# Kernel optimization log

Measured on AMD Instinct MI355X. Metric: run time of the kernel, lower is better.

The kernel has to match this reference:

```python
import jax, jax.numpy as jnp
import numpy as np

EPS = 1e-5

@jax.custom_vjp
def sign_ste(x):
    # binarize to {-1, +1}; sign(0) maps to +1 as in most binary-net impls
    return jnp.where(x >= 0, 1.0, -1.0).astype(x.dtype)

def _sign_fwd(x):
    return sign_ste(x), x

def _sign_bwd(x, g):
    # straight-through estimator with hardtanh clipping
    return (g * (jnp.abs(x) <= 1.0).astype(g.dtype),)

sign_ste.defvjp(_sign_fwd, _sign_bwd)


def setup_inputs() -> dict:
    key = jax.random.key(0)
    k1, k2, k3 = jax.random.split(key, 3)
    N, Cin, Cout = 65536, 1024, 1024
    return {
        "x": jax.random.normal(k1, (N, Cin), dtype=jnp.float32),
        "gamma": jnp.ones((Cin,), dtype=jnp.float32),
        "beta": jnp.zeros((Cin,), dtype=jnp.float32),
        "W": jax.random.normal(k2, (Cout, Cin), dtype=jnp.float32) * 0.03,
        "b": jnp.zeros((Cout,), dtype=jnp.float32),
        "scale": jnp.ones((Cout,), dtype=jnp.float32),
        "alpha": jnp.float32(0.25),
    }


def reference(x, gamma, beta, W, b, scale, alpha):
    # 1) BatchNorm1d centering (training-mode batch statistics over nodes)
    mu = jnp.mean(x, axis=0)
    var = jnp.var(x, axis=0)
    xh = (x - mu) * jax.lax.rsqrt(var + EPS) * gamma + beta
    # 2) STE binarize activations
    xq = sign_ste(xh)
    # 3) binary linear: sign(W) GEMM + bias  -> [N, Cout]
    wq = sign_ste(W)
    y = jnp.einsum('nc,oc->no', xq, wq) + b
    # 4) learned per-channel rescale
    y = y * scale
    # 5) PReLU
    return jnp.where(y > 0, y, alpha * y)
```

## Files before the change

### kernel.cpp

```cpp
#include <hip/hip_runtime.h>
#include <stdint.h>
#include <math.h>

#define NROWS 65536
#define CIN   1024
#define COUT  1024
#define KW    16
#define BN_EPS 1e-5

static constexpr size_t OFF_PSUM = 0;
static constexpr size_t OFF_PSQ  = 524288;
static constexpr size_t OFF_MU   = 1048576;
static constexpr size_t OFF_INV  = 1048576 + 4096;
static constexpr size_t OFF_WB   = 1048576 + 65536;
static constexpr size_t OFF_AB   = 1310720;

__global__ __launch_bounds__(256) void k_stats_partial(
    const float* __restrict__ x, double* __restrict__ psum, double* __restrict__ psq) {
  int c  = blockIdx.x * 256 + threadIdx.x;
  size_t r0 = (size_t)blockIdx.y * 1024;
  const float* p = x + r0 * CIN + c;
  double s = 0.0, q = 0.0;
  for (int r = 0; r < 1024; ++r) {
    double v = (double)p[(size_t)r * CIN];
    s += v;
    q = fma(v, v, q);
  }
  psum[(size_t)blockIdx.y * CIN + c] = s;
  psq [(size_t)blockIdx.y * CIN + c] = q;
}

__global__ __launch_bounds__(256) void k_stats_final(
    const double* __restrict__ psum, const double* __restrict__ psq,
    float* __restrict__ mu, float* __restrict__ inv) {
  int c = blockIdx.x * 256 + threadIdx.x;
  double s = 0.0, q = 0.0;
  for (int p = 0; p < 64; ++p) {
    s += psum[(size_t)p * CIN + c];
    q += psq [(size_t)p * CIN + c];
  }
  double mean = s / (double)NROWS;
  double var  = q / (double)NROWS - mean * mean;
  mu[c]  = (float)mean;
  inv[c] = (float)(1.0 / sqrt(var + (double)BN_EPS));
}

__global__ __launch_bounds__(256) void k_binarize_x(
    const float* __restrict__ x, const float* __restrict__ mu,
    const float* __restrict__ inv, const float* __restrict__ gamma,
    const float* __restrict__ beta, uint64_t* __restrict__ Abits) {
  int n    = blockIdx.x;
  int tid  = threadIdx.x;
  int lane = tid & 63;
  int wave = tid >> 6;
  const float* row = x + (size_t)n * CIN;
  #pragma unroll
  for (int j = 0; j < 4; ++j) {
    int c = j * 256 + tid;
    float xh = ((row[c] - mu[c]) * inv[c]) * gamma[c] + beta[c];
    uint64_t m = __ballot(xh >= 0.0f);
    if (lane == 0) Abits[(size_t)n * KW + j * 4 + wave] = m;
  }
}

__global__ __launch_bounds__(256) void k_binarize_w(
    const float* __restrict__ W, uint64_t* __restrict__ Wbits) {
  int o    = blockIdx.x;
  int tid  = threadIdx.x;
  int lane = tid & 63;
  int wave = tid >> 6;
  const float* row = W + (size_t)o * CIN;
  #pragma unroll
  for (int j = 0; j < 4; ++j) {
    int c = j * 256 + tid;
    uint64_t m = __ballot(row[c] >= 0.0f);
    if (lane == 0) Wbits[(size_t)o * KW + j * 4 + wave] = m;
  }
}

__global__ __launch_bounds__(256) void k_bingemm(
    const uint64_t* __restrict__ Abits, const uint64_t* __restrict__ Wbits,
    const float* __restrict__ bias, const float* __restrict__ scale,
    const float* __restrict__ alphaPtr, float* __restrict__ out) {
  int o = blockIdx.x * 256 + threadIdx.x;

  uint64_t B[KW];
  #pragma unroll
  for (int j = 0; j < KW; ++j) B[j] = Wbits[(size_t)o * KW + j];

  float alpha = alphaPtr[0];
  float sc = scale[o];
  float c2 = -2.0f * sc;
  float c1 = (1024.0f + bias[o]) * sc;

  int n0 = blockIdx.y * 64;
  for (int r = 0; r < 64; ++r) {
    int n = n0 + r;
    const uint64_t* A = Abits + (size_t)n * KW;
    int d0 = 0, d1 = 0, d2 = 0, d3 = 0;
    #pragma unroll
    for (int j = 0; j < KW; j += 4) {
      d0 += __popcll(A[j + 0] ^ B[j + 0]);
      d1 += __popcll(A[j + 1] ^ B[j + 1]);
      d2 += __popcll(A[j + 2] ^ B[j + 2]);
      d3 += __popcll(A[j + 3] ^ B[j + 3]);
    }
    int d = (d0 + d1) + (d2 + d3);
    float y = fmaf((float)d, c2, c1);
    out[(size_t)n * COUT + o] = y > 0.0f ? y : alpha * y;
  }
}

extern "C" void kernel_launch(void* const* d_in, const int* in_sizes, int n_in,
                              void* d_out, int out_size, void* d_ws, size_t ws_size,
                              hipStream_t stream) {
  const float* x     = (const float*)d_in[0];
  const float* gamma = (const float*)d_in[1];
  const float* beta  = (const float*)d_in[2];
  const float* W     = (const float*)d_in[3];
  const float* b     = (const float*)d_in[4];
  const float* scale = (const float*)d_in[5];
  const float* alpha = (const float*)d_in[6];
  float* out = (float*)d_out;

  char* ws = (char*)d_ws;
  double*   psum  = (double*)(ws + OFF_PSUM);
  double*   psq   = (double*)(ws + OFF_PSQ);
  float*    mu    = (float*)(ws + OFF_MU);
  float*    inv   = (float*)(ws + OFF_INV);
  uint64_t* Wbits = (uint64_t*)(ws + OFF_WB);
  uint64_t* Abits = (uint64_t*)(ws + OFF_AB);

  k_stats_partial<<<dim3(CIN / 256, NROWS / 1024), 256, 0, stream>>>(x, psum, psq);
  k_stats_final<<<dim3(CIN / 256), 256, 0, stream>>>(psum, psq, mu, inv);
  k_binarize_w<<<dim3(COUT), 256, 0, stream>>>(W, Wbits);
  k_binarize_x<<<dim3(NROWS), 256, 0, stream>>>(x, mu, inv, gamma, beta, Abits);
  k_bingemm<<<dim3(COUT / 256, NROWS / 64), 256, 0, stream>>>(
      Abits, Wbits, b, scale, alpha, out);
}
```

Measured before the change: 633.0 us.

## Vectorize stats and binarize kernels, use scalar constant loads for GEMM rows

```diff
diff --git a/kernel.cpp b/kernel.cpp
--- a/kernel.cpp
+++ b/kernel.cpp
@@ -5,109 +5,162 @@
 #define NROWS 65536
 #define CIN   1024
 #define COUT  1024
-#define KW    16
 #define BN_EPS 1e-5
 
+
 static constexpr size_t OFF_PSUM = 0;
-static constexpr size_t OFF_PSQ  = 524288;
-static constexpr size_t OFF_MU   = 1048576;
-static constexpr size_t OFF_INV  = 1048576 + 4096;
-static constexpr size_t OFF_WB   = 1048576 + 65536;
-static constexpr size_t OFF_AB   = 1310720;
+static constexpr size_t OFF_PSQ  = 2u * 1024 * 1024;
+static constexpr size_t OFF_MU   = 4u * 1024 * 1024;
+static constexpr size_t OFF_INV  = 4u * 1024 * 1024 + 4096;
+static constexpr size_t OFF_WB   = 5u * 1024 * 1024;
+static constexpr size_t OFF_AB   = 6u * 1024 * 1024;
+
+typedef uint64_t u64x2 __attribute__((ext_vector_type(2)));
+typedef uint32_t u32x4 __attribute__((ext_vector_type(4)));
+typedef const u32x4 __attribute__((address_space(4)))* c4p;
 
 __global__ __launch_bounds__(256) void k_stats_partial(
     const float* __restrict__ x, double* __restrict__ psum, double* __restrict__ psq) {
-  int c  = blockIdx.x * 256 + threadIdx.x;
-  size_t r0 = (size_t)blockIdx.y * 1024;
-  const float* p = x + r0 * CIN + c;
-  double s = 0.0, q = 0.0;
-  for (int r = 0; r < 1024; ++r) {
-    double v = (double)p[(size_t)r * CIN];
-    s += v;
-    q = fma(v, v, q);
+  int tid = threadIdx.x;
+  size_t r0 = (size_t)blockIdx.x * 256;
+  const float4* xp = (const float4*)x + r0 * 256 + tid;
+  double s0 = 0, s1 = 0, s2 = 0, s3 = 0;
+  double q0 = 0, q1 = 0, q2 = 0, q3 = 0;
+  for (int r = 0; r < 256; r += 8) {
+    float4 v[8];
+#pragma unroll
+    for (int u = 0; u < 8; ++u) v[u] = xp[(size_t)(r + u) * 256];
+#pragma unroll
+    for (int u = 0; u < 8; ++u) {
+      double a = (double)v[u].x, b = (double)v[u].y;
+      double c = (double)v[u].z, d = (double)v[u].w;
+      s0 += a; q0 = fma(a, a, q0);
+      s1 += b; q1 = fma(b, b, q1);
+      s2 += c; q2 = fma(c, c, q2);
+      s3 += d; q3 = fma(d, d, q3);
+    }
   }
-  psum[(size_t)blockIdx.y * CIN + c] = s;
-  psq [(size_t)blockIdx.y * CIN + c] = q;
+  size_t base = (size_t)blockIdx.x * CIN + (size_t)tid * 4;
+  double2* ps = (double2*)(psum + base);
+  ps[0] = make_double2(s0, s1);
+  ps[1] = make_double2(s2, s3);
+  double2* pq = (double2*)(psq + base);
+  pq[0] = make_double2(q0, q1);
+  pq[1] = make_double2(q2, q3);
 }
 
 __global__ __launch_bounds__(256) void k_stats_final(
     const double* __restrict__ psum, const double* __restrict__ psq,
     float* __restrict__ mu, float* __restrict__ inv) {
-  int c = blockIdx.x * 256 + threadIdx.x;
-  double s = 0.0, q = 0.0;
-  for (int p = 0; p < 64; ++p) {
-    s += psum[(size_t)p * CIN + c];
-    q += psq [(size_t)p * CIN + c];
+  __shared__ double sd[4][64];
+  __shared__ double sq[4][64];
+  int tid = threadIdx.x, lane = tid & 63, g = tid >> 6;
+  int col = blockIdx.x * 64 + lane;
+  double s = 0, q = 0;
+  for (int i = 0; i < 64; ++i) {
+    size_t chunk = (size_t)(g * 64 + i);
+    s += psum[chunk * CIN + col];
+    q += psq [chunk * CIN + col];
   }
-  double mean = s / (double)NROWS;
-  double var  = q / (double)NROWS - mean * mean;
-  mu[c]  = (float)mean;
-  inv[c] = (float)(1.0 / sqrt(var + (double)BN_EPS));
+  sd[g][lane] = s;
+  sq[g][lane] = q;
+  __syncthreads();
+  if (g == 0) {
+    s = sd[0][lane] + sd[1][lane] + sd[2][lane] + sd[3][lane];
+    q = sq[0][lane] + sq[1][lane] + sq[2][lane] + sq[3][lane];
+    double mean = s / (double)NROWS;
+    double var  = q / (double)NROWS - mean * mean;
+    mu[col]  = (float)mean;
+    inv[col] = (float)(1.0 / sqrt(var + (double)BN_EPS));
+  }
 }
 
 __global__ __launch_bounds__(256) void k_binarize_x(
     const float* __restrict__ x, const float* __restrict__ mu,
     const float* __restrict__ inv, const float* __restrict__ gamma,
     const float* __restrict__ beta, uint64_t* __restrict__ Abits) {
-  int n    = blockIdx.x;
-  int tid  = threadIdx.x;
-  int lane = tid & 63;
-  int wave = tid >> 6;
-  const float* row = x + (size_t)n * CIN;
-  #pragma unroll
-  for (int j = 0; j < 4; ++j) {
-    int c = j * 256 + tid;
-    float xh = ((row[c] - mu[c]) * inv[c]) * gamma[c] + beta[c];
-    uint64_t m = __ballot(xh >= 0.0f);
-    if (lane == 0) Abits[(size_t)n * KW + j * 4 + wave] = m;
+  int tid = threadIdx.x, lane = tid & 63, wv = tid >> 6;
+  float4 M  = ((const float4*)mu)[tid];
+  float4 I  = ((const float4*)inv)[tid];
+  float4 G  = ((const float4*)gamma)[tid];
+  float4 Bt = ((const float4*)beta)[tid];
+  size_t n0 = (size_t)blockIdx.x * 8;
+  const float4* xp = (const float4*)x + n0 * 256 + tid;
+  for (int r = 0; r < 8; ++r) {
+    float4 v = xp[(size_t)r * 256];
+    float h0 = ((v.x - M.x) * I.x) * G.x + Bt.x;
+    float h1 = ((v.y - M.y) * I.y) * G.y + Bt.y;
+    float h2 = ((v.z - M.z) * I.z) * G.z + Bt.z;
+    float h3 = ((v.w - M.w) * I.w) * G.w + Bt.w;
+    uint64_t b0 = __ballot(h0 >= 0.0f);
+    uint64_t b1 = __ballot(h1 >= 0.0f);
+    uint64_t b2 = __ballot(h2 >= 0.0f);
+    uint64_t b3 = __ballot(h3 >= 0.0f);
+    uint64_t t0 = b0, t1 = b1;
+    if (lane == 1) { t0 = b2; t1 = b3; }
+    if (lane < 2) {
+      u64x2 val; val.x = t0; val.y = t1;
+      *(u64x2*)(Abits + (n0 + r) * 16 + wv * 4 + lane * 2) = val;
+    }
   }
 }
 
 __global__ __launch_bounds__(256) void k_binarize_w(
     const float* __restrict__ W, uint64_t* __restrict__ Wbits) {
-  int o    = blockIdx.x;
-  int tid  = threadIdx.x;
-  int lane = tid & 63;
-  int wave = tid >> 6;
-  const float* row = W + (size_t)o * CIN;
-  #pragma unroll
-  for (int j = 0; j < 4; ++j) {
-    int c = j * 256 + tid;
-    uint64_t m = __ballot(row[c] >= 0.0f);
-    if (lane == 0) Wbits[(size_t)o * KW + j * 4 + wave] = m;
+  int tid = threadIdx.x, lane = tid & 63, wv = tid >> 6;
+  size_t o0 = (size_t)blockIdx.x * 8;
+  const float4* wp = (const float4*)W + o0 * 256 + tid;
+  for (int r = 0; r < 8; ++r) {
+    float4 v = wp[(size_t)r * 256];
+    uint64_t b0 = __ballot(v.x >= 0.0f);
+    uint64_t b1 = __ballot(v.y >= 0.0f);
+    uint64_t b2 = __ballot(v.z >= 0.0f);
+    uint64_t b3 = __ballot(v.w >= 0.0f);
+    uint64_t t0 = b0, t1 = b1;
+    if (lane == 1) { t0 = b2; t1 = b3; }
+    if (lane < 2) {
+      u64x2 val; val.x = t0; val.y = t1;
+      *(u64x2*)(Wbits + (o0 + r) * 16 + wv * 4 + lane * 2) = val;
+    }
   }
 }
 
 __global__ __launch_bounds__(256) void k_bingemm(
-    const uint64_t* __restrict__ Abits, const uint64_t* __restrict__ Wbits,
+    const uint32_t* __restrict__ Abits, const uint32_t* __restrict__ Wbits,
     const float* __restrict__ bias, const float* __restrict__ scale,
     const float* __restrict__ alphaPtr, float* __restrict__ out) {
-  int o = blockIdx.x * 256 + threadIdx.x;
+  int tid = threadIdx.x;
+  int o = blockIdx.x * 256 + tid;
 
-  uint64_t B[KW];
-  #pragma unroll
-  for (int j = 0; j < KW; ++j) B[j] = Wbits[(size_t)o * KW + j];
+  u32x4 B[8];
+  const u32x4* wp = (const u32x4*)(Wbits + (size_t)o * 32);
+#pragma unroll
+  for (int j = 0; j < 8; ++j) B[j] = wp[j];
 
   float alpha = alphaPtr[0];
   float sc = scale[o];
   float c2 = -2.0f * sc;
   float c1 = (1024.0f + bias[o]) * sc;
 
-  int n0 = blockIdx.y * 64;
+  size_t n0 = (size_t)blockIdx.y * 64;
+  c4p Ar = (c4p)(uintptr_t)(Abits + n0 * 32);
+  float* op = out + n0 * COUT + o;
+
   for (int r = 0; r < 64; ++r) {
-    int n = n0 + r;
-    const uint64_t* A = Abits + (size_t)n * KW;
     int d0 = 0, d1 = 0, d2 = 0, d3 = 0;
-    #pragma unroll
-    for (int j = 0; j < KW; j += 4) {
-      d0 += __popcll(A[j + 0] ^ B[j + 0]);
-      d1 += __popcll(A[j + 1] ^ B[j + 1]);
-      d2 += __popcll(A[j + 2] ^ B[j + 2]);
-      d3 += __popcll(A[j + 3] ^ B[j + 3]);
+#pragma unroll
+    for (int j = 0; j < 8; ++j) {
+      u32x4 a = Ar[j];
+      d0 += __builtin_popcount(a.x ^ B[j].x);
+      d1 += __builtin_popcount(a.y ^ B[j].y);
+      d2 += __builtin_popcount(a.z ^ B[j].z);
+      d3 += __builtin_popcount(a.w ^ B[j].w);
     }
+    Ar += 8;
     int d = (d0 + d1) + (d2 + d3);
     float y = fmaf((float)d, c2, c1);
-    out[(size_t)n * COUT + o] = y > 0.0f ? y : alpha * y;
+    *op = y > 0.0f ? y : alpha * y;
+    op += COUT;
   }
 }
 
@@ -131,10 +184,10 @@
   uint64_t* Wbits = (uint64_t*)(ws + OFF_WB);
   uint64_t* Abits = (uint64_t*)(ws + OFF_AB);
 
-  k_stats_partial<<<dim3(CIN / 256, NROWS / 1024), 256, 0, stream>>>(x, psum, psq);
-  k_stats_final<<<dim3(CIN / 256), 256, 0, stream>>>(psum, psq, mu, inv);
-  k_binarize_w<<<dim3(COUT), 256, 0, stream>>>(W, Wbits);
-  k_binarize_x<<<dim3(NROWS), 256, 0, stream>>>(x, mu, inv, gamma, beta, Abits);
+  k_stats_partial<<<dim3(NROWS / 256), 256, 0, stream>>>(x, psum, psq);
+  k_stats_final<<<dim3(CIN / 64), 256, 0, stream>>>(psum, psq, mu, inv);
+  k_binarize_w<<<dim3(COUT / 8), 256, 0, stream>>>(W, Wbits);
+  k_binarize_x<<<dim3(NROWS / 8), 256, 0, stream>>>(x, mu, inv, gamma, beta, Abits);
   k_bingemm<<<dim3(COUT / 256, NROWS / 64), 256, 0, stream>>>(
-      Abits, Wbits, b, scale, alpha, out);
+      (const uint32_t*)Abits, (const uint32_t*)Wbits, b, scale, alpha, out);
 }
```

Result: faster. 607.4 us (-4.1%).
